# Performance work log

Hardware: AMD Instinct MI355X
Metric: run time of the kernel (lower is better)

Reference implementation:

```python
import jax, jax.numpy as jnp
import numpy as np

T, D, E, I, K = 8192, 1024, 16, 2048, 4

def setup_inputs() -> dict:
    key = jax.random.key(0)
    k1, k2, k3, k4 = jax.random.split(key, 4)
    return {
        "hidden_states": jax.random.normal(k1, (T, D), dtype=jnp.float32),
        "router_logits": jax.random.normal(k2, (T, E), dtype=jnp.float32),
        "w13_weight": jax.random.normal(k3, (E, 2 * I, D), dtype=jnp.float32) * 0.01,
        "w2_weight": jax.random.normal(k4, (E, D, I), dtype=jnp.float32) * 0.01,
        "top_k": K,
    }

def reference(hidden_states, router_logits, w13_weight, w2_weight, top_k):
    x = hidden_states                      # [T, D]
    n_exp = w13_weight.shape[0]
    n_tok = x.shape[0]
    inter = w2_weight.shape[2]
    # --- router: softmax over all experts, top-k, renormalize ---
    probs = jax.nn.softmax(router_logits, axis=-1)          # [T, E]
    topk_w, topk_ids = jax.lax.top_k(probs, top_k)          # [T, K]
    topk_w = topk_w / jnp.sum(topk_w, axis=-1, keepdims=True)
    # dense combine weights: cw[t, e] = sum_k topk_w[t,k] * (topk_ids[t,k]==e)
    cw = jnp.zeros((n_tok, n_exp), dtype=x.dtype)
    cw = cw.at[jnp.arange(n_tok)[:, None], topk_ids].add(topk_w)  # [T, E]
    # --- experts: SwiGLU FFN per expert, weighted sum (scan keeps memory low) ---
    def body(acc, ewc):
        w13, w2, c = ewc                    # [2I, D], [D, I], [T]
        gate = x @ w13[:inter].T            # [T, I]
        up = x @ w13[inter:].T              # [T, I]
        h = jax.nn.silu(gate) * up          # [T, I]
        return acc + c[:, None] * (h @ w2.T), None
    out, _ = jax.lax.scan(body, jnp.zeros_like(x), (w13_weight, w2_weight, cw.T))
    return out
```

## Files before the change

kernel.cpp:

```cpp
#include <hip/hip_runtime.h>
#include <hip/hip_bf16.h>

#define T_TOK 8192
#define D_DIM 1024
#define E_NUM 16
#define I_DIM 2048
#define K_TOP 4
#define NPAIR (T_TOK * K_TOP)

typedef float f32x4 __attribute__((ext_vector_type(4)));
typedef __bf16 bf16x8 __attribute__((ext_vector_type(8)));
typedef unsigned short ushort8_t __attribute__((ext_vector_type(8)));

#define WS_X    0ull
#define WS_W13  (WS_X    + (size_t)T_TOK * D_DIM * 2)
#define WS_W2   (WS_W13  + (size_t)E_NUM * 2 * I_DIM * D_DIM * 2)
#define WS_H    (WS_W2   + (size_t)E_NUM * D_DIM * I_DIM * 2)
#define WS_TKID (WS_H    + (size_t)NPAIR * I_DIM * 2)
#define WS_TKW  (WS_TKID + (size_t)T_TOK * K_TOP * 4)
#define WS_PTOK (WS_TKW  + (size_t)T_TOK * K_TOP * 4)
#define WS_PW   (WS_PTOK + (size_t)NPAIR * 4)
#define WS_META (WS_PW   + (size_t)NPAIR * 4)

__device__ inline unsigned short f2bf(float f) {
    unsigned u = __builtin_bit_cast(unsigned, f);
    u += 0x7fffu + ((u >> 16) & 1u);
    return (unsigned short)(u >> 16);
}

__global__ void cvt_kernel(const float* __restrict__ in,
                           unsigned short* __restrict__ out, int n) {
    int idx = blockIdx.x * blockDim.x + threadIdx.x;
    int stride = gridDim.x * blockDim.x;
    for (int i = idx * 4; i < n; i += stride * 4) {
        float4 v = *(const float4*)(in + i);
        ushort4 o;
        o.x = f2bf(v.x); o.y = f2bf(v.y); o.z = f2bf(v.z); o.w = f2bf(v.w);
        *(ushort4*)(out + i) = o;
    }
}

__global__ void router_kernel(const float* __restrict__ logits,
                              int* __restrict__ tk_id, float* __restrict__ tk_w,
                              int* __restrict__ cnt) {
    int t = blockIdx.x * blockDim.x + threadIdx.x;
    if (t >= T_TOK) return;
    float l[E_NUM];
    const float4* lp = (const float4*)(logits + (size_t)t * E_NUM);
#pragma unroll
    for (int i = 0; i < 4; i++) {
        float4 v = lp[i];
        l[4 * i] = v.x; l[4 * i + 1] = v.y; l[4 * i + 2] = v.z; l[4 * i + 3] = v.w;
    }
    unsigned used = 0;
    int ids[K_TOP]; float vs[K_TOP];
#pragma unroll
    for (int k = 0; k < K_TOP; k++) {
        float best = -1e30f; int bi = 0;
#pragma unroll
        for (int e = 0; e < E_NUM; e++) {
            bool ok = !((used >> e) & 1u);
            if (ok && l[e] > best) { best = l[e]; bi = e; }
        }
        ids[k] = bi; vs[k] = best; used |= (1u << bi);
    }
    float m = vs[0];
    float s = 0.f;
#pragma unroll
    for (int k = 0; k < K_TOP; k++) { vs[k] = expf(vs[k] - m); s += vs[k]; }
    float inv = 1.f / s;
#pragma unroll
    for (int k = 0; k < K_TOP; k++) {
        tk_id[t * K_TOP + k] = ids[k];
        tk_w[t * K_TOP + k] = vs[k] * inv;
        atomicAdd(&cnt[ids[k]], 1);
    }
}

__global__ void offsets_kernel(const int* __restrict__ cnt,
                               int* __restrict__ off, int* __restrict__ cur) {
    if (threadIdx.x == 0 && blockIdx.x == 0) {
        int o = 0;
        for (int e = 0; e < E_NUM; e++) { off[e] = o; cur[e] = o; o += cnt[e]; }
    }
}

__global__ void scatter_kernel(const int* __restrict__ tk_id,
                               const float* __restrict__ tk_w,
                               int* __restrict__ cur,
                               int* __restrict__ p_tok, float* __restrict__ p_w) {
    int t = blockIdx.x * blockDim.x + threadIdx.x;
    if (t >= T_TOK) return;
#pragma unroll
    for (int k = 0; k < K_TOP; k++) {
        int e = tk_id[t * K_TOP + k];
        int pos = atomicAdd(&cur[e], 1);
        p_tok[pos] = t;
        p_w[pos] = tk_w[t * K_TOP + k];
    }
}

__global__ __launch_bounds__(256, 2) void gemm1_kernel(
    const unsigned short* __restrict__ xb, const unsigned short* __restrict__ w13,
    const int* __restrict__ cnt, const int* __restrict__ off,
    const int* __restrict__ p_tok, unsigned short* __restrict__ h) {
    int e = blockIdx.z;
    int cnt_e = cnt[e];
    int m0 = blockIdx.y * 128;
    if (m0 >= cnt_e) return;
    int n0 = blockIdx.x * 128;
    int base = off[e];

    __shared__ unsigned short As[128][40];
    __shared__ unsigned short Bg[128][40];
    __shared__ unsigned short Bu[128][40];
    __shared__ int toks[128];

    int tid = threadIdx.x;
    int lane = tid & 63, wid = tid >> 6;
    int wm = wid >> 1, wn = wid & 1;

    if (tid < 128) {
        int r = m0 + tid;
        toks[tid] = (r < cnt_e) ? p_tok[base + r] : -1;
    }
    __syncthreads();

    int sr = tid >> 1;
    int sc = (tid & 1) * 16;
    int atok = toks[sr];
    const unsigned short* w13e = w13 + (size_t)e * (2 * I_DIM) * D_DIM;
    const unsigned short* gRow = w13e + (size_t)(n0 + sr) * D_DIM;
    const unsigned short* uRow = w13e + (size_t)(I_DIM + n0 + sr) * D_DIM;
    const unsigned short* aRow = (atok >= 0) ? (xb + (size_t)atok * D_DIM) : (const unsigned short*)0;

    f32x4 accg[4][4], accu[4][4];
#pragma unroll
    for (int m = 0; m < 4; m++)
#pragma unroll
        for (int n = 0; n < 4; n++) {
            accg[m][n] = (f32x4){0.f, 0.f, 0.f, 0.f};
            accu[m][n] = (f32x4){0.f, 0.f, 0.f, 0.f};
        }

    for (int k0 = 0; k0 < D_DIM; k0 += 32) {
        ushort8_t av0 = {0,0,0,0,0,0,0,0}, av1 = {0,0,0,0,0,0,0,0};
        if (aRow) {
            av0 = *(const ushort8_t*)(aRow + k0 + sc);
            av1 = *(const ushort8_t*)(aRow + k0 + sc + 8);
        }
        ushort8_t g0 = *(const ushort8_t*)(gRow + k0 + sc);
        ushort8_t g1 = *(const ushort8_t*)(gRow + k0 + sc + 8);
        ushort8_t u0 = *(const ushort8_t*)(uRow + k0 + sc);
        ushort8_t u1 = *(const ushort8_t*)(uRow + k0 + sc + 8);
        *(ushort8_t*)&As[sr][sc]     = av0;
        *(ushort8_t*)&As[sr][sc + 8] = av1;
        *(ushort8_t*)&Bg[sr][sc]     = g0;
        *(ushort8_t*)&Bg[sr][sc + 8] = g1;
        *(ushort8_t*)&Bu[sr][sc]     = u0;
        *(ushort8_t*)&Bu[sr][sc + 8] = u1;
        __syncthreads();

        int fr = lane & 15, fk = (lane >> 4) * 8;
        bf16x8 a[4], bg[4], bu[4];
#pragma unroll
        for (int m = 0; m < 4; m++) a[m] = *(const bf16x8*)&As[wm * 64 + m * 16 + fr][fk];
#pragma unroll
        for (int n = 0; n < 4; n++) {
            bg[n] = *(const bf16x8*)&Bg[wn * 64 + n * 16 + fr][fk];
            bu[n] = *(const bf16x8*)&Bu[wn * 64 + n * 16 + fr][fk];
        }
#pragma unroll
        for (int m = 0; m < 4; m++)
#pragma unroll
            for (int n = 0; n < 4; n++) {
                accg[m][n] = __builtin_amdgcn_mfma_f32_16x16x32_bf16(a[m], bg[n], accg[m][n], 0, 0, 0);
                accu[m][n] = __builtin_amdgcn_mfma_f32_16x16x32_bf16(a[m], bu[n], accu[m][n], 0, 0, 0);
            }
        __syncthreads();
    }

    int fr = lane & 15, fq = lane >> 4;
#pragma unroll
    for (int m = 0; m < 4; m++) {
#pragma unroll
        for (int j = 0; j < 4; j++) {
            int rr = wm * 64 + m * 16 + fq * 4 + j;
            if (m0 + rr < cnt_e) {
                size_t hrow = (size_t)(base + m0 + rr) * I_DIM;
#pragma unroll
                for (int n = 0; n < 4; n++) {
                    float g = accg[m][n][j];
                    float u = accu[m][n][j];
                    float hh = (g / (1.f + __expf(-g))) * u;
                    h[hrow + n0 + wn * 64 + n * 16 + fr] = f2bf(hh);
                }
            }
        }
    }
}

__global__ __launch_bounds__(256, 2) void gemm2_kernel(
    const unsigned short* __restrict__ h, const unsigned short* __restrict__ w2,
    const int* __restrict__ cnt, const int* __restrict__ off,
    const int* __restrict__ p_tok, const float* __restrict__ p_w,
    float* __restrict__ out) {
    int e = blockIdx.z;
    int cnt_e = cnt[e];
    int m0 = blockIdx.y * 128;
    if (m0 >= cnt_e) return;
    int n0 = blockIdx.x * 128;
    int base = off[e];

    __shared__ unsigned short As[128][40];
    __shared__ unsigned short Bs[128][40];
    __shared__ int toks[128];
    __shared__ float pws[128];

    int tid = threadIdx.x;
    int lane = tid & 63, wid = tid >> 6;
    int wm = wid >> 1, wn = wid & 1;

    if (tid < 128) {
        int r = m0 + tid;
        toks[tid] = (r < cnt_e) ? p_tok[base + r] : 0;
        pws[tid]  = (r < cnt_e) ? p_w[base + r] : 0.f;
    }
    __syncthreads();

    int sr = tid >> 1;
    int sc = (tid & 1) * 16;
    bool arow_ok = (m0 + sr) < cnt_e;
    const unsigned short* aRow = h + (size_t)(base + m0 + sr) * I_DIM;
    const unsigned short* bRow = w2 + (size_t)e * D_DIM * I_DIM + (size_t)(n0 + sr) * I_DIM;

    f32x4 acc[4][4];
#pragma unroll
    for (int m = 0; m < 4; m++)
#pragma unroll
        for (int n = 0; n < 4; n++) acc[m][n] = (f32x4){0.f, 0.f, 0.f, 0.f};

    for (int k0 = 0; k0 < I_DIM; k0 += 32) {
        ushort8_t a0 = {0,0,0,0,0,0,0,0}, a1 = {0,0,0,0,0,0,0,0};
        if (arow_ok) {
            a0 = *(const ushort8_t*)(aRow + k0 + sc);
            a1 = *(const ushort8_t*)(aRow + k0 + sc + 8);
        }
        ushort8_t b0 = *(const ushort8_t*)(bRow + k0 + sc);
        ushort8_t b1 = *(const ushort8_t*)(bRow + k0 + sc + 8);
        *(ushort8_t*)&As[sr][sc]     = a0;
        *(ushort8_t*)&As[sr][sc + 8] = a1;
        *(ushort8_t*)&Bs[sr][sc]     = b0;
        *(ushort8_t*)&Bs[sr][sc + 8] = b1;
        __syncthreads();

        int fr = lane & 15, fk = (lane >> 4) * 8;
        bf16x8 a[4], b[4];
#pragma unroll
        for (int m = 0; m < 4; m++) a[m] = *(const bf16x8*)&As[wm * 64 + m * 16 + fr][fk];
#pragma unroll
        for (int n = 0; n < 4; n++) b[n] = *(const bf16x8*)&Bs[wn * 64 + n * 16 + fr][fk];
#pragma unroll
        for (int m = 0; m < 4; m++)
#pragma unroll
            for (int n = 0; n < 4; n++)
                acc[m][n] = __builtin_amdgcn_mfma_f32_16x16x32_bf16(a[m], b[n], acc[m][n], 0, 0, 0);
        __syncthreads();
    }

    int fr = lane & 15, fq = lane >> 4;
#pragma unroll
    for (int m = 0; m < 4; m++) {
#pragma unroll
        for (int j = 0; j < 4; j++) {
            int rr = wm * 64 + m * 16 + fq * 4 + j;
            if (m0 + rr < cnt_e) {
                int t = toks[rr];
                float w = pws[rr];
#pragma unroll
                for (int n = 0; n < 4; n++) {
                    atomicAdd(&out[(size_t)t * D_DIM + n0 + wn * 64 + n * 16 + fr],
                              acc[m][n][j] * w);
                }
            }
        }
    }
}

extern "C" void kernel_launch(void* const* d_in, const int* in_sizes, int n_in,
                              void* d_out, int out_size, void* d_ws, size_t ws_size,
                              hipStream_t stream) {
    const float* x      = (const float*)d_in[0];
    const float* logits = (const float*)d_in[1];
    const float* w13    = (const float*)d_in[2];
    const float* w2     = (const float*)d_in[3];
    float* out = (float*)d_out;
    char* ws = (char*)d_ws;

    unsigned short* xb   = (unsigned short*)(ws + WS_X);
    unsigned short* w13b = (unsigned short*)(ws + WS_W13);
    unsigned short* w2b  = (unsigned short*)(ws + WS_W2);
    unsigned short* hbuf = (unsigned short*)(ws + WS_H);
    int*   tk_id = (int*)(ws + WS_TKID);
    float* tk_w  = (float*)(ws + WS_TKW);
    int*   p_tok = (int*)(ws + WS_PTOK);
    float* p_w   = (float*)(ws + WS_PW);
    int* meta = (int*)(ws + WS_META);
    int* cnt = meta;
    int* cur = meta + 16;
    int* off = meta + 32;

    hipMemsetAsync(meta, 0, 32 * sizeof(int), stream);
    hipMemsetAsync(out, 0, (size_t)T_TOK * D_DIM * sizeof(float), stream);

    cvt_kernel<<<1024, 256, 0, stream>>>(x, xb, T_TOK * D_DIM);
    cvt_kernel<<<2048, 256, 0, stream>>>(w13, w13b, E_NUM * 2 * I_DIM * D_DIM);
    cvt_kernel<<<2048, 256, 0, stream>>>(w2, w2b, E_NUM * D_DIM * I_DIM);

    router_kernel<<<T_TOK / 256, 256, 0, stream>>>(logits, tk_id, tk_w, cnt);
    offsets_kernel<<<1, 64, 0, stream>>>(cnt, off, cur);
    scatter_kernel<<<T_TOK / 256, 256, 0, stream>>>(tk_id, tk_w, cur, p_tok, p_w);

    dim3 g1(I_DIM / 128, 64, E_NUM);
    gemm1_kernel<<<g1, 256, 0, stream>>>(xb, w13b, cnt, off, p_tok, hbuf);
    dim3 g2(D_DIM / 128, 64, E_NUM);
    gemm2_kernel<<<g2, 256, 0, stream>>>(hbuf, w2b, cnt, off, p_tok, p_w, out);
}
```

Measured before the change: 1.324 ms.

## Replace atomic scatter in down-projection with per-pair partials and combine kernel

The second GEMM can now write each (token, expert) row's weighted result contiguously into a per-pair partial buffer. A new combine kernel then sums the four partials for each token using a recorded pair index, which removes the float atomics and the output memset. This path is taken only when the workspace is large enough, and it adds a 128 MB partial buffer write plus a read pass. Both GEMMs also raise the launch_bounds occupancy hint from 2 to 4 blocks, which may force register spills.

```diff
diff --git a/kernel.cpp b/kernel.cpp
--- a/kernel.cpp
+++ b/kernel.cpp
@@ -21,6 +21,9 @@
 #define WS_PTOK (WS_TKW  + (size_t)T_TOK * K_TOP * 4)
 #define WS_PW   (WS_PTOK + (size_t)NPAIR * 4)
 #define WS_META (WS_PW   + (size_t)NPAIR * 4)
+#define WS_PAIR (WS_META + 256)
+#define WS_PART (WS_PAIR + (size_t)NPAIR * 4)
+#define WS_NEED_FULL (WS_PART + (size_t)NPAIR * D_DIM * 4)
 
 __device__ inline unsigned short f2bf(float f) {
     unsigned u = __builtin_bit_cast(unsigned, f);
@@ -88,7 +91,8 @@
 __global__ void scatter_kernel(const int* __restrict__ tk_id,
                                const float* __restrict__ tk_w,
                                int* __restrict__ cur,
-                               int* __restrict__ p_tok, float* __restrict__ p_w) {
+                               int* __restrict__ p_tok, float* __restrict__ p_w,
+                               int* __restrict__ pair_of) {
     int t = blockIdx.x * blockDim.x + threadIdx.x;
     if (t >= T_TOK) return;
 #pragma unroll
@@ -97,10 +101,11 @@
         int pos = atomicAdd(&cur[e], 1);
         p_tok[pos] = t;
         p_w[pos] = tk_w[t * K_TOP + k];
-    }
-}
-
-__global__ __launch_bounds__(256, 2) void gemm1_kernel(
+        pair_of[t * K_TOP + k] = pos;
+    }
+}
+
+__global__ __launch_bounds__(256, 4) void gemm1_kernel(
     const unsigned short* __restrict__ xb, const unsigned short* __restrict__ w13,
     const int* __restrict__ cnt, const int* __restrict__ off,
     const int* __restrict__ p_tok, unsigned short* __restrict__ h) {
@@ -200,11 +205,12 @@
     }
 }
 
-__global__ __launch_bounds__(256, 2) void gemm2_kernel(
+template<bool USE_ATOMIC>
+__global__ __launch_bounds__(256, 4) void gemm2_kernel(
     const unsigned short* __restrict__ h, const unsigned short* __restrict__ w2,
     const int* __restrict__ cnt, const int* __restrict__ off,
     const int* __restrict__ p_tok, const float* __restrict__ p_w,
-    float* __restrict__ out) {
+    float* __restrict__ dst) {
     int e = blockIdx.z;
     int cnt_e = cnt[e];
     int m0 = blockIdx.y * 128;
@@ -275,16 +281,38 @@
         for (int j = 0; j < 4; j++) {
             int rr = wm * 64 + m * 16 + fq * 4 + j;
             if (m0 + rr < cnt_e) {
-                int t = toks[rr];
                 float w = pws[rr];
 #pragma unroll
                 for (int n = 0; n < 4; n++) {
-                    atomicAdd(&out[(size_t)t * D_DIM + n0 + wn * 64 + n * 16 + fr],
-                              acc[m][n][j] * w);
+                    int col = n0 + wn * 64 + n * 16 + fr;
+                    float v = acc[m][n][j] * w;
+                    if (USE_ATOMIC) {
+                        atomicAdd(&dst[(size_t)toks[rr] * D_DIM + col], v);
+                    } else {
+                        dst[(size_t)(base + m0 + rr) * D_DIM + col] = v;
+                    }
                 }
             }
         }
     }
+}
+
+__global__ __launch_bounds__(256) void combine_kernel(
+    const float* __restrict__ part, const int* __restrict__ pair_of,
+    float* __restrict__ out) {
+    int t = blockIdx.x;
+    int c = threadIdx.x * 4;
+    int4 pr = *(const int4*)(pair_of + t * K_TOP);
+    float4 s0 = *(const float4*)(part + (size_t)pr.x * D_DIM + c);
+    float4 s1 = *(const float4*)(part + (size_t)pr.y * D_DIM + c);
+    float4 s2 = *(const float4*)(part + (size_t)pr.z * D_DIM + c);
+    float4 s3 = *(const float4*)(part + (size_t)pr.w * D_DIM + c);
+    float4 r;
+    r.x = (s0.x + s1.x) + (s2.x + s3.x);
+    r.y = (s0.y + s1.y) + (s2.y + s3.y);
+    r.z = (s0.z + s1.z) + (s2.z + s3.z);
+    r.w = (s0.w + s1.w) + (s2.w + s3.w);
+    *(float4*)(out + (size_t)t * D_DIM + c) = r;
 }
 
 extern "C" void kernel_launch(void* const* d_in, const int* in_sizes, int n_in,
@@ -309,9 +337,13 @@
     int* cnt = meta;
     int* cur = meta + 16;
     int* off = meta + 32;
+    int*   pair_of = (int*)(ws + WS_PAIR);
+    float* part    = (float*)(ws + WS_PART);
+
+    bool full = (ws_size >= WS_NEED_FULL);
 
     hipMemsetAsync(meta, 0, 32 * sizeof(int), stream);
-    hipMemsetAsync(out, 0, (size_t)T_TOK * D_DIM * sizeof(float), stream);
+    if (!full) hipMemsetAsync(out, 0, (size_t)T_TOK * D_DIM * sizeof(float), stream);
 
     cvt_kernel<<<1024, 256, 0, stream>>>(x, xb, T_TOK * D_DIM);
     cvt_kernel<<<2048, 256, 0, stream>>>(w13, w13b, E_NUM * 2 * I_DIM * D_DIM);
@@ -319,10 +351,16 @@
 
     router_kernel<<<T_TOK / 256, 256, 0, stream>>>(logits, tk_id, tk_w, cnt);
     offsets_kernel<<<1, 64, 0, stream>>>(cnt, off, cur);
-    scatter_kernel<<<T_TOK / 256, 256, 0, stream>>>(tk_id, tk_w, cur, p_tok, p_w);
+    scatter_kernel<<<T_TOK / 256, 256, 0, stream>>>(tk_id, tk_w, cur, p_tok, p_w, pair_of);
 
     dim3 g1(I_DIM / 128, 64, E_NUM);
     gemm1_kernel<<<g1, 256, 0, stream>>>(xb, w13b, cnt, off, p_tok, hbuf);
+
     dim3 g2(D_DIM / 128, 64, E_NUM);
-    gemm2_kernel<<<g2, 256, 0, stream>>>(hbuf, w2b, cnt, off, p_tok, p_w, out);
-}
+    if (full) {
+        gemm2_kernel<false><<<g2, 256, 0, stream>>>(hbuf, w2b, cnt, off, p_tok, p_w, part);
+        combine_kernel<<<T_TOK, 256, 0, stream>>>(part, pair_of, out);
+    } else {
+        gemm2_kernel<true><<<g2, 256, 0, stream>>>(hbuf, w2b, cnt, off, p_tok, p_w, out);
+    }
+}
```

After: 3.461 ms. 161% more time.
